# Performance work log

Hardware: AMD Instinct MI355X
Metric: run time of the kernel (lower is better)

## Reference

```python
import jax, jax.numpy as jnp
import numpy as np

B, S, D, H, DH = 2, 2048, 1024, 16, 64
EPS = 1e-6


def setup_inputs() -> dict:
    key = jax.random.key(0)
    k0, k1, k2 = jax.random.split(key, 3)
    x = jax.random.normal(k0, (B, S, D), dtype=jnp.float32)
    mask = jnp.ones((B, S), dtype=bool)
    # NeoX-style rotary angles: half-dim inverse freqs, duplicated to rot_dim=DH
    inv_freq = 1.0 / (10000.0 ** (jnp.arange(0, DH, 2, dtype=jnp.float32) / DH))  # [DH/2]
    ang = jnp.arange(S, dtype=jnp.float32)[:, None] * inv_freq[None, :]            # [S, DH/2]
    freqs = jnp.concatenate([ang, ang], axis=-1)                                    # [S, DH]
    W_qkv = jax.random.normal(k1, (3 * D, D), dtype=jnp.float32) * (D ** -0.5)
    W_out = jax.random.normal(k2, (D, D), dtype=jnp.float32) * (D ** -0.5)
    q_gamma = jnp.ones((DH,), jnp.float32)
    q_beta = jnp.zeros((DH,), jnp.float32)
    k_gamma = jnp.ones((DH,), jnp.float32)
    k_beta = jnp.zeros((DH,), jnp.float32)
    return {"x": x, "mask": mask, "freqs": freqs, "W_qkv": W_qkv, "W_out": W_out,
            "q_gamma": q_gamma, "q_beta": q_beta, "k_gamma": k_gamma, "k_beta": k_beta}


def _layernorm(t, g, b):
    mu = t.mean(-1, keepdims=True)
    var = t.var(-1, keepdims=True)
    return (t - mu) * jax.lax.rsqrt(var + EPS) * g + b


def _rotate_half(t):
    t1, t2 = jnp.split(t, 2, axis=-1)
    return jnp.concatenate([-t2, t1], axis=-1)


def reference(x, mask, freqs, W_qkv, W_out, q_gamma, q_beta, k_gamma, k_beta):
    b, s, d = x.shape
    # fused QKV projection + split into heads: b n (h d) -> b h n d
    qkv = x @ W_qkv.T                                   # [b, s, 3d]
    q, k, v = jnp.split(qkv, 3, axis=-1)
    to_heads = lambda t: t.reshape(b, s, H, DH).transpose(0, 2, 1, 3)
    q, k, v = to_heads(q), to_heads(k), to_heads(v)      # [b, h, s, dh]
    # qk layernorm
    q = _layernorm(q, q_gamma, q_beta)
    k = _layernorm(k, k_gamma, k_beta)
    # rotary embedding (fp32 path in the original; inputs already fp32)
    cos = jnp.cos(freqs)[None, None]                      # [1, 1, s, dh]
    sin = jnp.sin(freqs)[None, None]
    q = q * cos + _rotate_half(q) * sin
    k = k * cos + _rotate_half(k) * sin
    # mask construction: key padding mask 'b j -> b 1 1 j' combined with causal
    key_mask = mask[:, None, None, :]                     # [b, 1, 1, s]
    causal = jnp.tril(jnp.ones((s, s), dtype=bool))       # [s, s]
    comb = key_mask & causal[None, None]                  # [b, 1, s, s]
    row_masked = ~comb.any(axis=-1)                       # [b, 1, s]
    comb = comb.at[..., 0].set(comb[..., 0] | row_masked)
    # SDPA
    scale = DH ** -0.5
    scores = jnp.einsum('bhid,bhjd->bhij', q, k) * scale  # [b, h, s, s]
    scores = jnp.where(comb, scores, jnp.finfo(scores.dtype).min)
    attn = jax.nn.softmax(scores, axis=-1)
    out = jnp.einsum('bhij,bhjd->bhid', attn, v)          # [b, h, s, dh]
    out = jnp.where(row_masked[..., None], 0.0, out)
    # merge heads + output projection
    out = out.transpose(0, 2, 1, 3).reshape(b, s, d)
    return out @ W_out.T
```

## Files before the change

kernel.cpp:

```cpp
#include <hip/hip_runtime.h>
#include <hip/hip_bf16.h>
#include <cstdint>

typedef unsigned short u16;
typedef __attribute__((ext_vector_type(8))) short s16x8;
typedef __attribute__((ext_vector_type(4))) float f32x4;
typedef __attribute__((ext_vector_type(16))) float f32x16;
typedef __attribute__((ext_vector_type(4))) unsigned int u32x4;
typedef __attribute__((ext_vector_type(2))) unsigned int u32x2;
typedef __attribute__((ext_vector_type(4))) u16 u16x4;

#define LOG2E 1.44269504088896340736f

__device__ __forceinline__ u16 f2b(float f) {
  union { float f; unsigned u; } v; v.f = f;
  unsigned r = v.u + 0x7FFF + ((v.u >> 16) & 1);
  return (u16)(r >> 16);
}

__device__ __forceinline__ float b2f(u16 u) {
  union { unsigned u; float f; } v; v.u = ((unsigned)u) << 16;
  return v.f;
}

__device__ __forceinline__ void gload_lds16(const u16* g, u16* l) {
  __builtin_amdgcn_global_load_lds((const __attribute__((address_space(1))) void*)g,
                                   (__attribute__((address_space(3))) void*)l, 16, 0, 0);
}

__global__ void cvt_bf16(const float* __restrict__ in, u16* __restrict__ out, int n) {
  int i = blockIdx.x * blockDim.x + threadIdx.x;
  if (i < n) out[i] = f2b(in[i]);
}

__global__ void trig_tab(const float* __restrict__ f, float* __restrict__ c,
                         float* __restrict__ s, int n) {
  int i = blockIdx.x * blockDim.x + threadIdx.x;
  if (i < n) { c[i] = cosf(f[i]); s[i] = sinf(f[i]); }
}

__global__ __launch_bounds__(256) void gemm_bt(const u16* __restrict__ A, const u16* __restrict__ B,
                                               float* __restrict__ C, int M, int N, int K) {
  __shared__ u16 sA[128 * 64];
  __shared__ u16 sB[128 * 64];
  const int nbn = N >> 7;
  int bx = blockIdx.x % nbn, by = blockIdx.x / nbn;
  int tid = threadIdx.x, w = tid >> 6, lane = tid & 63;
  int wr = (w >> 1) * 64, wc = (w & 1) * 64;
  int lr = lane >> 3, lc = lane & 7;
  f32x4 acc[4][4] = {};
  size_t arow = (size_t)(by * 128) * K;
  size_t brow = (size_t)(bx * 128) * K;
  for (int k0 = 0; k0 < K; k0 += 64) {
    __syncthreads();
    for (int c = 0; c < 4; ++c) {
      int r = w * 32 + c * 8;
      gload_lds16(A + arow + (size_t)(r + lr) * K + k0 + lc * 8, &sA[r * 64]);
      gload_lds16(B + brow + (size_t)(r + lr) * K + k0 + lc * 8, &sB[r * 64]);
    }
    __syncthreads();
    for (int kk = 0; kk < 64; kk += 32) {
      s16x8 af[4], bf[4];
      int ro = lane & 15, ko = kk + (lane >> 4) * 8;
      for (int m = 0; m < 4; ++m) af[m] = *(const s16x8*)&sA[(wr + m * 16 + ro) * 64 + ko];
      for (int n = 0; n < 4; ++n) bf[n] = *(const s16x8*)&sB[(wc + n * 16 + ro) * 64 + ko];
      for (int m = 0; m < 4; ++m)
        for (int n = 0; n < 4; ++n)
          acc[m][n] = __builtin_amdgcn_mfma_f32_16x16x32_bf16(af[m], bf[n], acc[m][n], 0, 0, 0);
    }
  }
  int ro = lane & 15, rg = lane >> 4;
  for (int m = 0; m < 4; ++m)
    for (int n = 0; n < 4; ++n) {
      int row = by * 128 + wr + m * 16 + rg * 4;
      int col = bx * 128 + wc + n * 16 + ro;
      float* cp = C + (size_t)row * N + col;
      for (int r = 0; r < 4; ++r) cp[(size_t)r * N] = acc[m][n][r];
    }
}

__global__ __launch_bounds__(256) void ln_rope(const float* __restrict__ qkv,
    const float* __restrict__ cosT, const float* __restrict__ sinT,
    const float* __restrict__ qg, const float* __restrict__ qb,
    const float* __restrict__ kg, const float* __restrict__ kb,
    u16* __restrict__ qo, u16* __restrict__ ko, u16* __restrict__ vo) {
  int gw = (blockIdx.x * 256 + threadIdx.x) >> 6;
  int lane = threadIdx.x & 63;
  int h = gw & 15, bs = gw >> 4;
  int s = bs & 2047, b = bs >> 11;
  const float* row = qkv + (size_t)bs * 3072;
  float qv = row[h * 64 + lane];
  float kv = row[1024 + h * 64 + lane];
  float vv = row[2048 + h * 64 + lane];

  float s1q = qv, s2q = qv * qv, s1k = kv, s2k = kv * kv;
  for (int off = 1; off < 64; off <<= 1) {
    s1q += __shfl_xor(s1q, off, 64); s2q += __shfl_xor(s2q, off, 64);
    s1k += __shfl_xor(s1k, off, 64); s2k += __shfl_xor(s2k, off, 64);
  }
  float muq = s1q * (1.f / 64.f), varq = s2q * (1.f / 64.f) - muq * muq;
  float muk = s1k * (1.f / 64.f), vark = s2k * (1.f / 64.f) - muk * muk;
  float qn = (qv - muq) * rsqrtf(varq + 1e-6f) * qg[lane] + qb[lane];
  float kn = (kv - muk) * rsqrtf(vark + 1e-6f) * kg[lane] + kb[lane];

  float cs = cosT[s * 64 + lane], sn = sinT[s * 64 + lane];
  float qh = __shfl_xor(qn, 32, 64); qh = (lane < 32) ? -qh : qh;
  float kh = __shfl_xor(kn, 32, 64); kh = (lane < 32) ? -kh : kh;
  float qr = (qn * cs + qh * sn) * 0.125f;
  float kr = kn * cs + kh * sn;

  size_t oidx = ((size_t)((b * 16 + h) * 2048 + s)) * 64 + lane;
  qo[oidx] = f2b(qr); ko[oidx] = f2b(kr); vo[oidx] = f2b(vv);
}

__global__ __launch_bounds__(256) void transpose_v(const u16* __restrict__ vi, u16* __restrict__ vt) {
  __shared__ __align__(16) u16 tile[64][72];
  int bh = blockIdx.x >> 5, st = blockIdx.x & 31;
  int t = threadIdx.x;
  const u16* src = vi + ((size_t)bh * 2048 + st * 64) * 64;
  int r = t & 63, c = (t >> 6) * 16;
  *(s16x8*)&tile[r][c]     = *(const s16x8*)(src + r * 64 + c);
  *(s16x8*)&tile[r][c + 8] = *(const s16x8*)(src + r * 64 + c + 8);
  __syncthreads();
  int dh = t & 63, so = (t >> 6) * 16;
  alignas(16) u16 buf[16];
  #pragma unroll
  for (int j = 0; j < 16; ++j) buf[j] = tile[so + j][dh];
  u16* dst = vt + ((size_t)bh * 64 + dh) * 2048 + st * 64 + so;
  *(s16x8*)dst       = *(const s16x8*)&buf[0];
  *(s16x8*)(dst + 8) = *(const s16x8*)&buf[8];
}

__global__ __launch_bounds__(256) void attn_fwd6(const u16* __restrict__ qp, const u16* __restrict__ kp,
                                                 const u16* __restrict__ vtp, u16* __restrict__ op) {
  __shared__ u16 sO[8][64][32];
  __shared__ float sM[8][32], sL[8][32];
  int bid = blockIdx.x;
  int xcd = bid & 7, j = bid >> 3;
  int bh = 4 * xcd + (j >> 5), pr = j & 31;
  int tid = threadIdx.x, w = tid >> 6, l = tid & 63;
  int ql = l & 31, h5 = l >> 5;
  const int A = pr, Bs = 63 - pr;
  int b = bh >> 4, h = bh & 15;
  const u16* qptr = qp + (size_t)bh * 2048 * 64;
  const u16* kptr = kp + (size_t)bh * 2048 * 64;
  const u16* vptr = vtp + (size_t)bh * 64 * 2048;

  s16x8 qfA[4], qfB[4];
  {
    const u16* qrA = qptr + (size_t)(A * 32 + ql) * 64 + h5 * 8;
    const u16* qrB = qptr + (size_t)(Bs * 32 + ql) * 64 + h5 * 8;
    #pragma unroll
    for (int t = 0; t < 4; ++t) { qfA[t] = *(const s16x8*)(qrA + 16 * t);
                                  qfB[t] = *(const s16x8*)(qrB + 16 * t); }
  }
  f32x16 oA0 = {}, oA1 = {}, oB0 = {}, oB1 = {};
  float mA = -INFINITY, lA = 0.f, mB = -INFINITY, lB = 0.f;

  auto tile = [&](const s16x8* qf, float& m, float& lsum, f32x16& o0, f32x16& o1,
                  s16x8 k0, s16x8 k1, s16x8 k2, s16x8 k3,
                  s16x8 v00, s16x8 v01, s16x8 v10, s16x8 v11, int kt, int strip) {
    f32x16 sc = {};
    sc = __builtin_amdgcn_mfma_f32_32x32x16_bf16(k0, qf[0], sc, 0, 0, 0);
    sc = __builtin_amdgcn_mfma_f32_32x32x16_bf16(k1, qf[1], sc, 0, 0, 0);
    sc = __builtin_amdgcn_mfma_f32_32x32x16_bf16(k2, qf[2], sc, 0, 0, 0);
    sc = __builtin_amdgcn_mfma_f32_32x32x16_bf16(k3, qf[3], sc, 0, 0, 0);

    if (kt == strip) {
      #pragma unroll
      for (int r = 0; r < 16; ++r) {
        int kloc = (r & 3) + 8 * (r >> 2) + 4 * h5;
        sc[r] = (kloc > ql) ? -INFINITY : sc[r];
      }
    }
    float t8[8], t4[4];
    #pragma unroll
    for (int i = 0; i < 8; ++i) t8[i] = fmaxf(sc[2 * i], sc[2 * i + 1]);
    #pragma unroll
    for (int i = 0; i < 4; ++i) t4[i] = fmaxf(t8[2 * i], t8[2 * i + 1]);
    float mx = fmaxf(fmaxf(t4[0], t4[1]), fmaxf(t4[2], t4[3]));
    mx = fmaxf(mx, __shfl_xor(mx, 32, 64));

    if (__any(mx > m)) {
      float mn = fmaxf(m, mx);
      float alpha = __builtin_amdgcn_exp2f((m - mn) * LOG2E);
      #pragma unroll
      for (int r = 0; r < 16; ++r) { o0[r] *= alpha; o1[r] *= alpha; }
      lsum *= alpha;
      m = mn;
    }
    float rs = 0.f;
    #pragma unroll
    for (int r = 0; r < 16; ++r) {
      float p = __builtin_amdgcn_exp2f((sc[r] - m) * LOG2E);
      sc[r] = p; rs += p;
    }
    rs += __shfl_xor(rs, 32, 64);
    lsum += rs;

    unsigned wd[8];
    #pragma unroll
    for (int i = 0; i < 8; ++i)
      asm("v_cvt_pk_bf16_f32 %0, %1, %2" : "=v"(wd[i]) : "v"(sc[2 * i]), "v"(sc[2 * i + 1]));
    u32x2 r02 = __builtin_amdgcn_permlane32_swap(wd[0], wd[2], false, false);
    u32x2 r13 = __builtin_amdgcn_permlane32_swap(wd[1], wd[3], false, false);
    u32x2 r46 = __builtin_amdgcn_permlane32_swap(wd[4], wd[6], false, false);
    u32x2 r57 = __builtin_amdgcn_permlane32_swap(wd[5], wd[7], false, false);
    u32x4 t0v = {r02[0], r13[0], r02[1], r13[1]};
    u32x4 t1v = {r46[0], r57[0], r46[1], r57[1]};
    s16x8 pa0 = __builtin_bit_cast(s16x8, t0v);
    s16x8 pa1 = __builtin_bit_cast(s16x8, t1v);

    o0 = __builtin_amdgcn_mfma_f32_32x32x16_bf16(v00, pa0, o0, 0, 0, 0);
    o0 = __builtin_amdgcn_mfma_f32_32x32x16_bf16(v01, pa1, o0, 0, 0, 0);
    o1 = __builtin_amdgcn_mfma_f32_32x32x16_bf16(v10, pa0, o1, 0, 0, 0);
    o1 = __builtin_amdgcn_mfma_f32_32x32x16_bf16(v11, pa1, o1, 0, 0, 0);
  };

  for (int kt = w; kt <= Bs; kt += 4) {
    const u16* kr = kptr + (size_t)(kt * 32 + ql) * 64 + h5 * 8;
    s16x8 k0 = *(const s16x8*)(kr);
    s16x8 k1 = *(const s16x8*)(kr + 16);
    s16x8 k2 = *(const s16x8*)(kr + 32);
    s16x8 k3 = *(const s16x8*)(kr + 48);
    const u16* vr = vptr + (size_t)ql * 2048 + kt * 32 + h5 * 8;
    s16x8 v00 = *(const s16x8*)(vr);
    s16x8 v01 = *(const s16x8*)(vr + 16);
    s16x8 v10 = *(const s16x8*)(vr + 32 * 2048);
    s16x8 v11 = *(const s16x8*)(vr + 32 * 2048 + 16);

    tile(qfB, mB, lB, oB0, oB1, k0, k1, k2, k3, v00, v01, v10, v11, kt, Bs);
    if (kt <= A)
      tile(qfA, mA, lA, oA0, oA1, k0, k1, k2, k3, v00, v01, v10, v11, kt, A);
  }

  if (h5 == 0) {
    sM[w * 2 + 0][ql] = mA; sL[w * 2 + 0][ql] = lA;
    sM[w * 2 + 1][ql] = mB; sL[w * 2 + 1][ql] = lB;
  }
  #pragma unroll
  for (int r = 0; r < 16; ++r) {
    int dh = (r & 3) + 8 * (r >> 2) + 4 * h5;
    sO[w * 2 + 0][dh][ql]      = f2b(oA0[r]);
    sO[w * 2 + 0][dh + 32][ql] = f2b(oA1[r]);
    sO[w * 2 + 1][dh][ql]      = f2b(oB0[r]);
    sO[w * 2 + 1][dh + 32][ql] = f2b(oB1[r]);
  }
  __syncthreads();

  {
    int q = tid & 31, dg = tid >> 5;
    #pragma unroll
    for (int s = 0; s < 2; ++s) {
      float m0 = sM[0 * 2 + s][q], m1 = sM[1 * 2 + s][q];
      float m2 = sM[2 * 2 + s][q], m3 = sM[3 * 2 + s][q];
      float mg = fmaxf(fmaxf(m0, m1), fmaxf(m2, m3));
      float e0 = __builtin_amdgcn_exp2f((m0 - mg) * LOG2E);
      float e1 = __builtin_amdgcn_exp2f((m1 - mg) * LOG2E);
      float e2 = __builtin_amdgcn_exp2f((m2 - mg) * LOG2E);
      float e3 = __builtin_amdgcn_exp2f((m3 - mg) * LOG2E);
      float lg = e0 * sL[0 * 2 + s][q] + e1 * sL[1 * 2 + s][q]
               + e2 * sL[2 * 2 + s][q] + e3 * sL[3 * 2 + s][q];
      float inv = 1.f / lg;
      alignas(16) u16 ob[8];
      #pragma unroll
      for (int jj = 0; jj < 8; ++jj) {
        int dh = dg * 8 + jj;
        float acc = e0 * b2f(sO[0 * 2 + s][dh][q]) + e1 * b2f(sO[1 * 2 + s][dh][q])
                  + e2 * b2f(sO[2 * 2 + s][dh][q]) + e3 * b2f(sO[3 * 2 + s][dh][q]);
        ob[jj] = f2b(acc * inv);
      }
      int q0s = (s ? Bs : A) * 32;
      u16* dst = op + ((size_t)(b * 2048 + q0s + q)) * 1024 + h * 64 + dg * 8;
      *(u16x4*)dst       = *(const u16x4*)&ob[0];
      *(u16x4*)(dst + 4) = *(const u16x4*)&ob[4];
    }
  }
}

extern "C" void kernel_launch(void* const* d_in, const int* in_sizes, int n_in,
                              void* d_out, int out_size, void* d_ws, size_t ws_size,
                              hipStream_t stream) {
  const float* x     = (const float*)d_in[0];
  const float* freqs = (const float*)d_in[2];
  const float* Wqkv  = (const float*)d_in[3];
  const float* Wout  = (const float*)d_in[4];
  const float* qg    = (const float*)d_in[5];
  const float* qb    = (const float*)d_in[6];
  const float* kg    = (const float*)d_in[7];
  const float* kb    = (const float*)d_in[8];
  float* out = (float*)d_out;

  u16* xb    = (u16*)d_ws;
  u16* wqkvb = xb + 4194304;
  u16* woutb = wqkvb + 3145728;
  float* cosT = (float*)(woutb + 1048576);
  float* sinT = cosT + 131072;
  float* qkv  = sinT + 131072;
  u16* qo = (u16*)(qkv + 12582912);
  u16* ko = qo + 4194304;
  u16* vo = ko + 4194304;
  u16* ao = vo + 4194304;
  u16* vt = (u16*)qkv;

  cvt_bf16<<<(4194304 + 255) / 256, 256, 0, stream>>>(x, xb, 4194304);
  cvt_bf16<<<(3145728 + 255) / 256, 256, 0, stream>>>(Wqkv, wqkvb, 3145728);
  cvt_bf16<<<(1048576 + 255) / 256, 256, 0, stream>>>(Wout, woutb, 1048576);
  trig_tab<<<(131072 + 255) / 256, 256, 0, stream>>>(freqs, cosT, sinT, 131072);

  gemm_bt<<<(4096 / 128) * (3072 / 128), 256, 0, stream>>>(xb, wqkvb, qkv, 4096, 3072, 1024);
  ln_rope<<<65536 / 4, 256, 0, stream>>>(qkv, cosT, sinT, qg, qb, kg, kb, qo, ko, vo);
  transpose_v<<<32 * 32, 256, 0, stream>>>(vo, vt);
  attn_fwd6<<<1024, 256, 0, stream>>>(qo, ko, vt, ao);
  gemm_bt<<<(4096 / 128) * (1024 / 128), 256, 0, stream>>>(ao, woutb, out, 4096, 1024, 1024);
}
```

Before: 261.6 us.

## Fuse QKV GEMM with LayerNorm+RoPE epilogue, merge prep kernels, swizzle GEMM blocks

The four conversion and trig-table kernels become one vectorized grid-stride prep kernel that writes interleaved cos/sin pairs. The QKV GEMM now applies per-head LayerNorm, rotary embedding and the q scale in its epilogue and writes bf16 q/k/v directly, so the fp32 qkv intermediate and the separate ln_rope pass are gone. GEMM block indices are swizzled across XCDs, and the attention MFMA sections are wrapped in s_setprio raises. The fused epilogue uses cross-lane shuffles and scattered 2-byte stores, which may coalesce less well than the old row-wise writes.

```diff
diff --git a/kernel.cpp b/kernel.cpp
--- a/kernel.cpp
+++ b/kernel.cpp
@@ -28,15 +28,27 @@
                                    (__attribute__((address_space(3))) void*)l, 16, 0, 0);
 }
 
-__global__ void cvt_bf16(const float* __restrict__ in, u16* __restrict__ out, int n) {
-  int i = blockIdx.x * blockDim.x + threadIdx.x;
-  if (i < n) out[i] = f2b(in[i]);
-}
-
-__global__ void trig_tab(const float* __restrict__ f, float* __restrict__ c,
-                         float* __restrict__ s, int n) {
-  int i = blockIdx.x * blockDim.x + threadIdx.x;
-  if (i < n) { c[i] = cosf(f[i]); s[i] = sinf(f[i]); }
+__global__ __launch_bounds__(256) void prep(const float* __restrict__ x, const float* __restrict__ wqkv,
+                                            const float* __restrict__ wout, const float* __restrict__ freqs,
+                                            u16* __restrict__ xb, u16* __restrict__ wqkvb,
+                                            u16* __restrict__ woutb, float2* __restrict__ trig) {
+  const int N1 = 1048576, N2 = 786432, N3 = 262144, NT = 131072;
+  const int TOT = N1 + N2 + N3 + NT;
+  for (int i = blockIdx.x * 256 + threadIdx.x; i < TOT; i += gridDim.x * 256) {
+    if (i < N1 + N2 + N3) {
+      const float4* src; u16* dst; int j = i;
+      if (i < N1)            { src = (const float4*)x;    dst = xb; }
+      else if (i < N1 + N2)  { src = (const float4*)wqkv; dst = wqkvb; j = i - N1; }
+      else                   { src = (const float4*)wout; dst = woutb; j = i - N1 - N2; }
+      float4 v = src[j];
+      u16x4 o = { f2b(v.x), f2b(v.y), f2b(v.z), f2b(v.w) };
+      *(u16x4*)(dst + 4 * j) = o;
+    } else {
+      int j = i - (N1 + N2 + N3);
+      float f = freqs[j];
+      trig[j] = make_float2(cosf(f), sinf(f));
+    }
+  }
 }
 
 __global__ __launch_bounds__(256) void gemm_bt(const u16* __restrict__ A, const u16* __restrict__ B,
@@ -44,7 +56,9 @@
   __shared__ u16 sA[128 * 64];
   __shared__ u16 sB[128 * 64];
   const int nbn = N >> 7;
-  int bx = blockIdx.x % nbn, by = blockIdx.x / nbn;
+  int nwg = gridDim.x;
+  int swz = (blockIdx.x & 7) * (nwg >> 3) + (blockIdx.x >> 3);
+  int bx = swz % nbn, by = swz / nbn;
   int tid = threadIdx.x, w = tid >> 6, lane = tid & 63;
   int wr = (w >> 1) * 64, wc = (w & 1) * 64;
   int lr = lane >> 3, lc = lane & 7;
@@ -79,38 +93,93 @@
     }
 }
 
-__global__ __launch_bounds__(256) void ln_rope(const float* __restrict__ qkv,
-    const float* __restrict__ cosT, const float* __restrict__ sinT,
+__global__ __launch_bounds__(256) void gemm_qkv_lnrope(
+    const u16* __restrict__ A, const u16* __restrict__ B, const float2* __restrict__ trig,
     const float* __restrict__ qg, const float* __restrict__ qb,
     const float* __restrict__ kg, const float* __restrict__ kb,
     u16* __restrict__ qo, u16* __restrict__ ko, u16* __restrict__ vo) {
-  int gw = (blockIdx.x * 256 + threadIdx.x) >> 6;
-  int lane = threadIdx.x & 63;
-  int h = gw & 15, bs = gw >> 4;
-  int s = bs & 2047, b = bs >> 11;
-  const float* row = qkv + (size_t)bs * 3072;
-  float qv = row[h * 64 + lane];
-  float kv = row[1024 + h * 64 + lane];
-  float vv = row[2048 + h * 64 + lane];
-
-  float s1q = qv, s2q = qv * qv, s1k = kv, s2k = kv * kv;
-  for (int off = 1; off < 64; off <<= 1) {
-    s1q += __shfl_xor(s1q, off, 64); s2q += __shfl_xor(s2q, off, 64);
-    s1k += __shfl_xor(s1k, off, 64); s2k += __shfl_xor(s2k, off, 64);
-  }
-  float muq = s1q * (1.f / 64.f), varq = s2q * (1.f / 64.f) - muq * muq;
-  float muk = s1k * (1.f / 64.f), vark = s2k * (1.f / 64.f) - muk * muk;
-  float qn = (qv - muq) * rsqrtf(varq + 1e-6f) * qg[lane] + qb[lane];
-  float kn = (kv - muk) * rsqrtf(vark + 1e-6f) * kg[lane] + kb[lane];
-
-  float cs = cosT[s * 64 + lane], sn = sinT[s * 64 + lane];
-  float qh = __shfl_xor(qn, 32, 64); qh = (lane < 32) ? -qh : qh;
-  float kh = __shfl_xor(kn, 32, 64); kh = (lane < 32) ? -kh : kh;
-  float qr = (qn * cs + qh * sn) * 0.125f;
-  float kr = kn * cs + kh * sn;
-
-  size_t oidx = ((size_t)((b * 16 + h) * 2048 + s)) * 64 + lane;
-  qo[oidx] = f2b(qr); ko[oidx] = f2b(kr); vo[oidx] = f2b(vv);
+  const int K = 1024;
+  __shared__ u16 sA[128 * 64];
+  __shared__ u16 sB[128 * 64];
+  int nwg = gridDim.x;
+  int swz = (blockIdx.x & 7) * (nwg >> 3) + (blockIdx.x >> 3);
+  int bx = swz % 24, by = swz / 24;
+  int tid = threadIdx.x, w = tid >> 6, lane = tid & 63;
+  int wr = (w >> 1) * 64, wc = (w & 1) * 64;
+  int lr = lane >> 3, lc = lane & 7;
+  f32x4 acc[4][4] = {};
+  size_t arow = (size_t)(by * 128) * K;
+  size_t brow = (size_t)(bx * 128) * K;
+  for (int k0 = 0; k0 < K; k0 += 64) {
+    __syncthreads();
+    for (int c = 0; c < 4; ++c) {
+      int r = w * 32 + c * 8;
+      gload_lds16(A + arow + (size_t)(r + lr) * K + k0 + lc * 8, &sA[r * 64]);
+      gload_lds16(B + brow + (size_t)(r + lr) * K + k0 + lc * 8, &sB[r * 64]);
+    }
+    __syncthreads();
+    for (int kk = 0; kk < 64; kk += 32) {
+      s16x8 af[4], bf[4];
+      int ro = lane & 15, ko = kk + (lane >> 4) * 8;
+      for (int m = 0; m < 4; ++m) af[m] = *(const s16x8*)&sA[(wr + m * 16 + ro) * 64 + ko];
+      for (int n = 0; n < 4; ++n) bf[n] = *(const s16x8*)&sB[(wc + n * 16 + ro) * 64 + ko];
+      for (int m = 0; m < 4; ++m)
+        for (int n = 0; n < 4; ++n)
+          acc[m][n] = __builtin_amdgcn_mfma_f32_16x16x32_bf16(af[m], bf[n], acc[m][n], 0, 0, 0);
+    }
+  }
+  int ro = lane & 15, rg = lane >> 4;
+  int gc0 = bx * 128 + wc;
+  int sec = gc0 >> 10;
+  int h = (gc0 & 1023) >> 6;
+  if (sec == 2) {
+    #pragma unroll
+    for (int m = 0; m < 4; ++m)
+      #pragma unroll
+      for (int r = 0; r < 4; ++r) {
+        int row = by * 128 + wr + m * 16 + rg * 4 + r;
+        int s = row & 2047, bb = row >> 11;
+        u16* dst = vo + ((size_t)((bb * 16 + h) * 2048 + s)) * 64;
+        #pragma unroll
+        for (int n = 0; n < 4; ++n) dst[n * 16 + ro] = f2b(acc[m][n][r]);
+      }
+  } else {
+    const float* gmm = sec ? kg : qg;
+    const float* bet = sec ? kb : qb;
+    float gv[4], bv[4];
+    #pragma unroll
+    for (int n = 0; n < 4; ++n) { gv[n] = gmm[n * 16 + ro]; bv[n] = bet[n * 16 + ro]; }
+    float qscale = sec == 0 ? 0.125f : 1.0f;
+    u16* base = sec == 0 ? qo : ko;
+    #pragma unroll
+    for (int m = 0; m < 4; ++m)
+      #pragma unroll
+      for (int r = 0; r < 4; ++r) {
+        float v0 = acc[m][0][r], v1 = acc[m][1][r], v2 = acc[m][2][r], v3 = acc[m][3][r];
+        float s1 = v0 + v1 + v2 + v3;
+        float s2 = v0 * v0 + v1 * v1 + v2 * v2 + v3 * v3;
+        #pragma unroll
+        for (int off = 1; off < 16; off <<= 1) {
+          s1 += __shfl_xor(s1, off, 64);
+          s2 += __shfl_xor(s2, off, 64);
+        }
+        float mu = s1 * (1.f / 64.f), var = s2 * (1.f / 64.f) - mu * mu;
+        float rr = rsqrtf(var + 1e-6f);
+        float nrm[4];
+        #pragma unroll
+        for (int n = 0; n < 4; ++n) nrm[n] = (acc[m][n][r] - mu) * rr * gv[n] + bv[n];
+        int row = by * 128 + wr + m * 16 + rg * 4 + r;
+        int s = row & 2047, bb = row >> 11;
+        const float2* tr = trig + (size_t)s * 64;
+        u16* dst = base + ((size_t)((bb * 16 + h) * 2048 + s)) * 64;
+        #pragma unroll
+        for (int n = 0; n < 4; ++n) {
+          float2 cs = tr[n * 16 + ro];
+          float rot = (n < 2) ? -nrm[n + 2] : nrm[n - 2];
+          dst[n * 16 + ro] = f2b((nrm[n] * cs.x + rot * cs.y) * qscale);
+        }
+      }
+  }
 }
 
 __global__ __launch_bounds__(256) void transpose_v(const u16* __restrict__ vi, u16* __restrict__ vt) {
@@ -131,7 +200,7 @@
   *(s16x8*)(dst + 8) = *(const s16x8*)&buf[8];
 }
 
-__global__ __launch_bounds__(256) void attn_fwd6(const u16* __restrict__ qp, const u16* __restrict__ kp,
+__global__ __launch_bounds__(256) void attn_fwd8(const u16* __restrict__ qp, const u16* __restrict__ kp,
                                                  const u16* __restrict__ vtp, u16* __restrict__ op) {
   __shared__ u16 sO[8][64][32];
   __shared__ float sM[8][32], sL[8][32];
@@ -161,10 +230,12 @@
                   s16x8 k0, s16x8 k1, s16x8 k2, s16x8 k3,
                   s16x8 v00, s16x8 v01, s16x8 v10, s16x8 v11, int kt, int strip) {
     f32x16 sc = {};
+    __builtin_amdgcn_s_setprio(1);
     sc = __builtin_amdgcn_mfma_f32_32x32x16_bf16(k0, qf[0], sc, 0, 0, 0);
     sc = __builtin_amdgcn_mfma_f32_32x32x16_bf16(k1, qf[1], sc, 0, 0, 0);
     sc = __builtin_amdgcn_mfma_f32_32x32x16_bf16(k2, qf[2], sc, 0, 0, 0);
     sc = __builtin_amdgcn_mfma_f32_32x32x16_bf16(k3, qf[3], sc, 0, 0, 0);
+    __builtin_amdgcn_s_setprio(0);
 
     if (kt == strip) {
       #pragma unroll
@@ -211,10 +282,12 @@
     s16x8 pa0 = __builtin_bit_cast(s16x8, t0v);
     s16x8 pa1 = __builtin_bit_cast(s16x8, t1v);
 
+    __builtin_amdgcn_s_setprio(1);
     o0 = __builtin_amdgcn_mfma_f32_32x32x16_bf16(v00, pa0, o0, 0, 0, 0);
     o0 = __builtin_amdgcn_mfma_f32_32x32x16_bf16(v01, pa1, o0, 0, 0, 0);
     o1 = __builtin_amdgcn_mfma_f32_32x32x16_bf16(v10, pa0, o1, 0, 0, 0);
     o1 = __builtin_amdgcn_mfma_f32_32x32x16_bf16(v11, pa1, o1, 0, 0, 0);
+    __builtin_amdgcn_s_setprio(0);
   };
 
   for (int kt = w; kt <= Bs; kt += 4) {
@@ -294,23 +367,16 @@
   u16* xb    = (u16*)d_ws;
   u16* wqkvb = xb + 4194304;
   u16* woutb = wqkvb + 3145728;
-  float* cosT = (float*)(woutb + 1048576);
-  float* sinT = cosT + 131072;
-  float* qkv  = sinT + 131072;
-  u16* qo = (u16*)(qkv + 12582912);
+  float2* trig2 = (float2*)(woutb + 1048576);
+  u16* qo = (u16*)(trig2 + 131072);
   u16* ko = qo + 4194304;
   u16* vo = ko + 4194304;
   u16* ao = vo + 4194304;
-  u16* vt = (u16*)qkv;
-
-  cvt_bf16<<<(4194304 + 255) / 256, 256, 0, stream>>>(x, xb, 4194304);
-  cvt_bf16<<<(3145728 + 255) / 256, 256, 0, stream>>>(Wqkv, wqkvb, 3145728);
-  cvt_bf16<<<(1048576 + 255) / 256, 256, 0, stream>>>(Wout, woutb, 1048576);
-  trig_tab<<<(131072 + 255) / 256, 256, 0, stream>>>(freqs, cosT, sinT, 131072);
-
-  gemm_bt<<<(4096 / 128) * (3072 / 128), 256, 0, stream>>>(xb, wqkvb, qkv, 4096, 3072, 1024);
-  ln_rope<<<65536 / 4, 256, 0, stream>>>(qkv, cosT, sinT, qg, qb, kg, kb, qo, ko, vo);
+  u16* vt = ao + 4194304;
+
+  prep<<<2048, 256, 0, stream>>>(x, Wqkv, Wout, freqs, xb, wqkvb, woutb, trig2);
+  gemm_qkv_lnrope<<<24 * 32, 256, 0, stream>>>(xb, wqkvb, trig2, qg, qb, kg, kb, qo, ko, vo);
   transpose_v<<<32 * 32, 256, 0, stream>>>(vo, vt);
-  attn_fwd6<<<1024, 256, 0, stream>>>(qo, ko, vt, ao);
+  attn_fwd8<<<1024, 256, 0, stream>>>(qo, ko, vt, ao);
   gemm_bt<<<(4096 / 128) * (1024 / 128), 256, 0, stream>>>(ao, woutb, out, 4096, 1024, 1024);
 }
```

Result: faster. 238.5 us (-8.8%).
